# Optimization experiments

Measured on AMD Instinct MI355X. Metric: run time of the kernel, lower is better.

Reference implementation:

```python
import jax, jax.numpy as jnp
import numpy as np

N_SU = 8
DATA_DIM = N_SU * N_SU - 1  # 63
BATCH = 1048576


def _gell_mann(n):
    """Generalized Gell-Mann matrices of su(n), Tr(L_a L_b) = 2 delta_ab."""
    mats = []
    for j in range(n):
        for k in range(j + 1, n):
            m = np.zeros((n, n), dtype=np.complex128); m[j, k] = 1.0; m[k, j] = 1.0
            mats.append(m)
            m = np.zeros((n, n), dtype=np.complex128); m[j, k] = -1.0j; m[k, j] = 1.0j
            mats.append(m)
    for l in range(1, n):
        m = np.zeros((n, n), dtype=np.complex128)
        c = np.sqrt(2.0 / (l * (l + 1)))
        for j in range(l):
            m[j, j] = c
        m[l, l] = -l * c
        mats.append(m)
    return np.stack(mats)


def _structure_const(n):
    """f_abc = Tr([L_a,L_b]L_c)/(4i), d_abc = Tr({L_a,L_b}L_c)/4 (both real)."""
    L = _gell_mann(n)                                  # (D, n, n)
    P = np.einsum('aij,bjk->abik', L, L)               # L_a L_b
    comm = P - P.transpose(1, 0, 2, 3)
    anti = P + P.transpose(1, 0, 2, 3)
    f = (np.einsum('abik,cki->abc', comm, L) / 4.0j).real
    d = (np.einsum('abik,cki->abc', anti, L) / 4.0).real
    return f.astype(np.float32), d.astype(np.float32)

F_CONST, D_CONST = _structure_const(N_SU)              # (D, D, D) each, compile-time constants
TRI = np.stack(np.triu_indices(DATA_DIM, 0))           # incl. diagonal
TRI1 = np.stack(np.triu_indices(DATA_DIM, 1))          # strict upper


def setup_inputs() -> dict:
    key = jax.random.key(0)
    k1, k2, k3, k4, k5 = jax.random.split(key, 5)
    D = DATA_DIM
    return {
        'x': jax.random.normal(k1, (BATCH, D), dtype=jnp.float32),
        'r_x': jax.random.uniform(k2, (D * (D + 1) // 2,), dtype=jnp.float32),
        'r_y': jax.random.uniform(k3, (D * (D - 1) // 2,), dtype=jnp.float32),
        'N': jax.random.uniform(k4, (1,), dtype=jnp.float32),
        'omega': jax.random.uniform(k5, (D,), dtype=jnp.float32),
    }


def _forward(x, r_x, r_y, N, omega):
    f = jnp.asarray(F_CONST)
    d = jnp.asarray(D_CONST)
    D = DATA_DIM
    # NOTE: faithful to the torch source, where `v_x = v_y = torch.zeros(...)`
    # aliases ONE tensor: r_y overwrites r_x on the strict upper triangle and
    # v_x is v_y, which makes c_im exactly zero.
    v = jnp.zeros((D, D), dtype=x.dtype)
    v = v.at[TRI[0], TRI[1]].set(r_x)
    v = v.at[TRI1[0], TRI1[1]].set(r_y)
    v_x = v
    v_y = v
    c_re = v_x.T @ v_x + v_y.T @ v_y                   # einsum('ki,kj->ij', v, v) x2
    c_re = c_re / jnp.trace(c_re)
    c_im = v_x.T @ v_y - v_y.T @ v_x                   # exactly zero (aliasing)
    c_re = N * c_re

    # Precompute the small (D,D) superoperator coefficient matrices once, then
    # apply them to the batch with plain matmuls (bn,mn->bm).
    A1 = jnp.einsum('mjk,ij->mik', f, c_re)
    M_re1 = jnp.einsum('mik,nik->mn', A1, f)           # 'mjk,nik,ij->mn'
    A2 = jnp.einsum('mik,ij->mjk', f, c_re)
    M_re2 = jnp.einsum('mjk,njk->mn', A2, f)           # 'mik,njk,ij->mn'
    B1 = jnp.einsum('mjk,ij->mik', f, c_im)
    M_im1 = jnp.einsum('mik,nik->mn', B1, d)
    B2 = jnp.einsum('mik,ij->mjk', f, c_im)
    M_im2 = jnp.einsum('mjk,njk->mn', B2, d)
    M = -2.0 * M_re1 - 2.0 * M_re2 - 2.0 * M_im1 + 2.0 * M_im2

    d_super_x = x @ M.T                                 # (B, D)
    H = 8.0 * jnp.einsum('kij,k->ij', f, omega)
    h_commutator_x = x @ H.T                            # 'kij,k,bj->bi'
    tr_id = -8.0 * jnp.einsum('imj,ij->m', f, c_im)     # (D,), zero here

    S_x = h_commutator_x + d_super_x
    T_x = x + tr_id
    L_x = S_x + T_x
    return x + 0.01 * L_x


def reference(x, r_x, r_y, N, omega):
    return _forward(x, r_x, r_y, N, omega)
```

## Files before the change

### kernel.cpp

```cpp
#include <hip/hip_runtime.h>
#include <hip/hip_bf16.h>

#define DD 63
#define DD2 (DD * DD)
#define NSU 8

typedef __attribute__((ext_vector_type(8))) short short8;
typedef __attribute__((ext_vector_type(4))) float f32x4;

__device__ float  g_F[DD2 * DD];
__device__ float  g_B[DD * DD2];
__device__ float  g_cc[DD2];
__device__ float  g_scale;
__device__ unsigned short g_Gb[64 * 64];

__device__ __forceinline__ unsigned short f2bf(float f) {
    union { float f; unsigned u; } v; v.f = f;
    unsigned r = v.u + 0x7FFFu + ((v.u >> 16) & 1u);
    return (unsigned short)(r >> 16);
}

__device__ __forceinline__ void fill_L(int a, float (*re)[NSU], float (*im)[NSU]) {
    if (a < 56) {
        int p = a >> 1;
        int j = 0, rem = p;
        while (rem >= 7 - j) { rem -= 7 - j; ++j; }
        int k = j + 1 + rem;
        if ((a & 1) == 0) { re[j][k] = 1.f; re[k][j] = 1.f; }
        else             { im[j][k] = -1.f; im[k][j] = 1.f; }
    } else {
        int l = a - 55;
        float c = sqrtf(2.f / (float)(l * (l + 1)));
        for (int j = 0; j < l; ++j) re[j][j] = c;
        re[l][l] = -(float)l * c;
    }
}

__global__ __launch_bounds__(256) void setup_kernel(const float* __restrict__ r_x,
                                                    const float* __restrict__ r_y,
                                                    const float* __restrict__ Np) {
    const int t = threadIdx.x;
    if (blockIdx.x < DD) {
        const int a = blockIdx.x;
        __shared__ float Ar[NSU][NSU], Ai[NSU][NSU];
        __shared__ float Br[4][NSU][NSU], Bi[4][NSU][NSU];
        __shared__ float Cr[4][NSU][NSU], Ci[4][NSU][NSU];
        const int w = t >> 6, lane = t & 63;
        const int r = lane >> 3, c = lane & 7;
        if (t < 64) { Ar[r][c] = 0.f; Ai[r][c] = 0.f; }
        __syncthreads();
        if (t == 0) fill_L(a, Ar, Ai);
        __syncthreads();
        for (int rb = 0; rb < 16; ++rb) {
            const int b = rb * 4 + w;
            const bool act = (b < DD);
            if (act) { Br[w][r][c] = 0.f; Bi[w][r][c] = 0.f; }
            __syncthreads();
            if (act && lane == 0) fill_L(b, Br[w], Bi[w]);
            __syncthreads();
            if (act) {
                float pr = 0.f, pi = 0.f, qr = 0.f, qi = 0.f;
                #pragma unroll
                for (int k = 0; k < NSU; ++k) {
                    pr += Ar[r][k] * Br[w][k][c] - Ai[r][k] * Bi[w][k][c];
                    pi += Ar[r][k] * Bi[w][k][c] + Ai[r][k] * Br[w][k][c];
                    qr += Br[w][r][k] * Ar[k][c] - Bi[w][r][k] * Ai[k][c];
                    qi += Br[w][r][k] * Ai[k][c] + Bi[w][r][k] * Ar[k][c];
                }
                Cr[w][r][c] = pr - qr;
                Ci[w][r][c] = pi - qi;
            }
            __syncthreads();
            if (act && lane < DD) {
                float im;
                if (lane < 56) {
                    int p = lane >> 1;
                    int j = 0, rem = p;
                    while (rem >= 7 - j) { rem -= 7 - j; ++j; }
                    int k = j + 1 + rem;
                    if ((lane & 1) == 0) im = Ci[w][j][k] + Ci[w][k][j];
                    else                 im = Cr[w][j][k] - Cr[w][k][j];
                } else {
                    int l = lane - 55;
                    float cd = sqrtf(2.f / (float)(l * (l + 1)));
                    float s = 0.f;
                    for (int j = 0; j < l; ++j) s += Ci[w][j][j];
                    im = cd * s - (float)l * cd * Ci[w][l][l];
                }
                g_F[(a * DD + b) * DD + lane] = 0.25f * im;
            }
            __syncthreads();
        }
    } else {
        __shared__ float v[DD2];
        __shared__ float ccs[DD2];
        for (int idx = t; idx < DD2; idx += 256) {
            int i = idx / DD, j = idx % DD;
            float val = 0.f;
            if (j > i)       val = r_y[62 * i - (i * (i - 1)) / 2 + (j - i - 1)];
            else if (j == i) val = r_x[63 * i - (i * (i - 1)) / 2];
            v[idx] = val;
        }
        __syncthreads();
        for (int idx = t; idx < DD2; idx += 256) {
            int i = idx / DD, j = idx % DD;
            float s = 0.f;
            for (int k = 0; k < DD; ++k) s = fmaf(v[k * DD + i], v[k * DD + j], s);
            ccs[idx] = s;
            g_cc[idx] = s;
        }
        __syncthreads();
        if (t == 0) {
            float tr = 0.f;
            for (int i = 0; i < DD; ++i) tr += ccs[i * DD + i];
            g_scale = Np[0] / tr;
        }
    }
}

__global__ __launch_bounds__(256) void buildB_kernel() {
    __shared__ float scc[DD2];
    __shared__ float sf[DD2];
    const int t = threadIdx.x;
    const int n = blockIdx.x;
    for (int idx = t; idx < DD2; idx += 256) {
        scc[idx] = g_cc[idx];
        sf[idx]  = g_F[n * DD2 + idx];
    }
    __syncthreads();
    for (int idx = t; idx < DD2; idx += 256) {
        const int j = idx / DD, k = idx % DD;
        float s = 0.f;
        for (int i = 0; i < DD; ++i) s = fmaf(scc[i * DD + j], sf[i * DD + k], s);
        g_B[n * DD2 + idx] = s;
    }
}

__global__ __launch_bounds__(64) void buildKt_kernel(const float* __restrict__ omega) {
    const int m = blockIdx.x >> 6;
    const int n = blockIdx.x & 63;
    const int lane = threadIdx.x;
    if (m >= DD || n >= DD) {
        if (lane == 0) g_Gb[m * 64 + n] = 0;
        return;
    }
    const float* __restrict__ Fm = g_F + m * DD2;
    const float* __restrict__ Bn = g_B + n * DD2;
    float p = 0.f;
    for (int idx = lane; idx < DD2; idx += 64) p = fmaf(Fm[idx], Bn[idx], p);
    float h = (lane < DD) ? g_F[lane * DD2 + m * DD + n] * omega[lane] : 0.f;
    #pragma unroll
    for (int off = 32; off > 0; off >>= 1) {
        p += __shfl_down(p, off);
        h += __shfl_down(h, off);
    }
    if (lane == 0)
        g_Gb[m * 64 + n] = f2bf(0.01f * (-4.f * g_scale * p + 8.f * h)
                                + ((m == n) ? 1.01f : 0.f));
}

__global__ __launch_bounds__(256) void apply_kernel(const float* __restrict__ x,
                                                    float* __restrict__ out,
                                                    int ntiles, int nwaves) {
    __shared__ float slab[4][16 * 64];
    const int t = threadIdx.x;
    const int w = t >> 6, lane = t & 63;
    const int mrow = lane & 15, q = lane >> 4;
    float* __restrict__ S = slab[w];

    const short8* __restrict__ gG = (const short8*)g_Gb;
    short8 bfrag[2][4];
    #pragma unroll
    for (int kt = 0; kt < 2; ++kt)
        #pragma unroll
        for (int nt = 0; nt < 4; ++nt)
            bfrag[kt][nt] = gG[(nt * 16 + mrow) * 8 + kt * 4 + q];

    if (lane < 16) S[lane * 64 + (((15 ^ lane) << 2) | 3)] = 0.f;

    int soff[4][4];
    #pragma unroll
    for (int i = 0; i < 4; ++i) {
        const int f = i * 64 + lane;
        #pragma unroll
        for (int j = 0; j < 4; ++j) {
            const int e = 4 * f + j;
            const int r = e / 63, c = e - r * 63;
            soff[i][j] = r * 64 + ((((c >> 2) ^ r) << 2) | (c & 3));
        }
    }
    const bool act3 = (lane < 60);

    int tile = blockIdx.x * 4 + w;
    if (tile >= ntiles) return;

    float4 ld[4];
    {
        const float4* __restrict__ gp = (const float4*)(x + (size_t)tile * (16 * DD));
        ld[0] = gp[lane]; ld[1] = gp[lane + 64]; ld[2] = gp[lane + 128];
        if (act3) ld[3] = gp[lane + 192];
    }

    while (true) {
        #pragma unroll
        for (int i = 0; i < 3; ++i) {
            S[soff[i][0]] = ld[i].x; S[soff[i][1]] = ld[i].y;
            S[soff[i][2]] = ld[i].z; S[soff[i][3]] = ld[i].w;
        }
        if (act3) {
            S[soff[3][0]] = ld[3].x; S[soff[3][1]] = ld[3].y;
            S[soff[3][2]] = ld[3].z; S[soff[3][3]] = ld[3].w;
        }
        const size_t tb = (size_t)tile * (16 * DD);
        const int next = tile + nwaves;

        float va[2][8];
        #pragma unroll
        for (int kt = 0; kt < 2; ++kt) {
            const int c0 = 8 * kt + 2 * q;
            *(float4*)&va[kt][0] = *(const float4*)&S[mrow * 64 + (((c0    ) ^ mrow) << 2)];
            *(float4*)&va[kt][4] = *(const float4*)&S[mrow * 64 + (((c0 + 1) ^ mrow) << 2)];
        }

        if (next < ntiles) {
            const float4* __restrict__ gp = (const float4*)(x + (size_t)next * (16 * DD));
            ld[0] = gp[lane]; ld[1] = gp[lane + 64]; ld[2] = gp[lane + 128];
            if (act3) ld[3] = gp[lane + 192];
        }

        short8 af[2];
        #pragma unroll
        for (int kt = 0; kt < 2; ++kt)
            #pragma unroll
            for (int j = 0; j < 8; ++j) {
                __hip_bfloat16 h = __float2bfloat16(va[kt][j]);
                af[kt][j] = *reinterpret_cast<short*>(&h);
            }

        f32x4 acc[4] = {{0.f,0.f,0.f,0.f},{0.f,0.f,0.f,0.f},
                        {0.f,0.f,0.f,0.f},{0.f,0.f,0.f,0.f}};
        #pragma unroll
        for (int nt = 0; nt < 4; ++nt) {
            acc[nt] = __builtin_amdgcn_mfma_f32_16x16x32_bf16(af[0], bfrag[0][nt], acc[nt], 0, 0, 0);
            acc[nt] = __builtin_amdgcn_mfma_f32_16x16x32_bf16(af[1], bfrag[1][nt], acc[nt], 0, 0, 0);
        }

        #pragma unroll
        for (int nt = 0; nt < 4; ++nt) {
            const int ocol = nt * 16 + mrow;
            if (ocol < DD) {
                #pragma unroll
                for (int r = 0; r < 4; ++r) {
                    const int orow = q * 4 + r;
                    S[orow * 64 + ((((ocol >> 2) ^ orow) << 2) | (ocol & 3))] = acc[nt][r];
                }
            }
        }

        #pragma unroll
        for (int i = 0; i < 3; ++i) {
            float4 o;
            o.x = S[soff[i][0]]; o.y = S[soff[i][1]];
            o.z = S[soff[i][2]]; o.w = S[soff[i][3]];
            ((float4*)(out + tb))[i * 64 + lane] = o;
        }
        if (act3) {
            float4 o;
            o.x = S[soff[3][0]]; o.y = S[soff[3][1]];
            o.z = S[soff[3][2]]; o.w = S[soff[3][3]];
            ((float4*)(out + tb))[192 + lane] = o;
        }

        if (next >= ntiles) break;
        tile = next;
    }
}

extern "C" void kernel_launch(void* const* d_in, const int* in_sizes, int n_in,
                              void* d_out, int out_size, void* d_ws, size_t ws_size,
                              hipStream_t stream) {
    const float* x     = (const float*)d_in[0];
    const float* r_x   = (const float*)d_in[1];
    const float* r_y   = (const float*)d_in[2];
    const float* Np    = (const float*)d_in[3];
    const float* omega = (const float*)d_in[4];
    float* out = (float*)d_out;

    const int rows = in_sizes[0] / DD;
    const int ntiles = rows / 16;
    const int ablocks = 2048;
    const int nwaves = ablocks * 4;

    setup_kernel<<<DD + 1, 256, 0, stream>>>(r_x, r_y, Np);
    buildB_kernel<<<DD, 256, 0, stream>>>();
    buildKt_kernel<<<64 * 64, 64, 0, stream>>>(omega);
    apply_kernel<<<ablocks, 256, 0, stream>>>(x, out, ntiles, nwaves);
}
```

Before: 180.3 us.

## Parallelize setup over (a,b) pairs and double-buffer x prefetch in apply

Splits the setup kernel so each structure-constant pair (a,b) and each column of the c matrix gets its own small block, instead of 64 blocks looping serially. The global trace/scale is now recomputed inside buildKt from the diagonal of g_cc, which removes a serial reduction step. The apply kernel keeps two register tile buffers so it prefetches two tiles ahead, giving more loads in flight at the cost of extra registers. Note that the diagonal read uses g_cc[lane*64], which matches i*63+i only because the row stride is 63 and 64 = 63+1.

```diff
diff --git a/kernel.cpp b/kernel.cpp
--- a/kernel.cpp
+++ b/kernel.cpp
@@ -11,7 +11,6 @@
 __device__ float  g_F[DD2 * DD];
 __device__ float  g_B[DD * DD2];
 __device__ float  g_cc[DD2];
-__device__ float  g_scale;
 __device__ unsigned short g_Gb[64 * 64];
 
 __device__ __forceinline__ unsigned short f2bf(float f) {
@@ -36,84 +35,63 @@
     }
 }
 
-__global__ __launch_bounds__(256) void setup_kernel(const float* __restrict__ r_x,
-                                                    const float* __restrict__ r_y,
-                                                    const float* __restrict__ Np) {
+__global__ __launch_bounds__(64) void setup1_kernel(const float* __restrict__ r_x,
+                                                    const float* __restrict__ r_y) {
     const int t = threadIdx.x;
-    if (blockIdx.x < DD) {
-        const int a = blockIdx.x;
-        __shared__ float Ar[NSU][NSU], Ai[NSU][NSU];
-        __shared__ float Br[4][NSU][NSU], Bi[4][NSU][NSU];
-        __shared__ float Cr[4][NSU][NSU], Ci[4][NSU][NSU];
-        const int w = t >> 6, lane = t & 63;
-        const int r = lane >> 3, c = lane & 7;
-        if (t < 64) { Ar[r][c] = 0.f; Ai[r][c] = 0.f; }
+    if (blockIdx.x < DD2) {
+        __shared__ float Ar[NSU][NSU], Ai[NSU][NSU], Br[NSU][NSU], Bi[NSU][NSU];
+        __shared__ float Cr[NSU][NSU], Ci[NSU][NSU];
+        const int a = blockIdx.x / DD, b = blockIdx.x % DD;
+        const int r = t >> 3, c = t & 7;
+        Ar[r][c] = 0.f; Ai[r][c] = 0.f; Br[r][c] = 0.f; Bi[r][c] = 0.f;
         __syncthreads();
         if (t == 0) fill_L(a, Ar, Ai);
-        __syncthreads();
-        for (int rb = 0; rb < 16; ++rb) {
-            const int b = rb * 4 + w;
-            const bool act = (b < DD);
-            if (act) { Br[w][r][c] = 0.f; Bi[w][r][c] = 0.f; }
-            __syncthreads();
-            if (act && lane == 0) fill_L(b, Br[w], Bi[w]);
-            __syncthreads();
-            if (act) {
-                float pr = 0.f, pi = 0.f, qr = 0.f, qi = 0.f;
-                #pragma unroll
-                for (int k = 0; k < NSU; ++k) {
-                    pr += Ar[r][k] * Br[w][k][c] - Ai[r][k] * Bi[w][k][c];
-                    pi += Ar[r][k] * Bi[w][k][c] + Ai[r][k] * Br[w][k][c];
-                    qr += Br[w][r][k] * Ar[k][c] - Bi[w][r][k] * Ai[k][c];
-                    qi += Br[w][r][k] * Ai[k][c] + Bi[w][r][k] * Ar[k][c];
-                }
-                Cr[w][r][c] = pr - qr;
-                Ci[w][r][c] = pi - qi;
+        if (t == 1) fill_L(b, Br, Bi);
+        __syncthreads();
+        float pr = 0.f, pi = 0.f, qr = 0.f, qi = 0.f;
+        #pragma unroll
+        for (int k = 0; k < NSU; ++k) {
+            pr += Ar[r][k] * Br[k][c] - Ai[r][k] * Bi[k][c];
+            pi += Ar[r][k] * Bi[k][c] + Ai[r][k] * Br[k][c];
+            qr += Br[r][k] * Ar[k][c] - Bi[r][k] * Ai[k][c];
+            qi += Br[r][k] * Ai[k][c] + Bi[r][k] * Ar[k][c];
+        }
+        Cr[r][c] = pr - qr;
+        Ci[r][c] = pi - qi;
+        __syncthreads();
+        if (t < DD) {
+            float im;
+            if (t < 56) {
+                int p = t >> 1;
+                int j = 0, rem = p;
+                while (rem >= 7 - j) { rem -= 7 - j; ++j; }
+                int k = j + 1 + rem;
+                if ((t & 1) == 0) im = Ci[j][k] + Ci[k][j];
+                else              im = Cr[j][k] - Cr[k][j];
+            } else {
+                int l = t - 55;
+                float cd = sqrtf(2.f / (float)(l * (l + 1)));
+                float s = 0.f;
+                for (int j = 0; j < l; ++j) s += Ci[j][j];
+                im = cd * s - (float)l * cd * Ci[l][l];
             }
-            __syncthreads();
-            if (act && lane < DD) {
-                float im;
-                if (lane < 56) {
-                    int p = lane >> 1;
-                    int j = 0, rem = p;
-                    while (rem >= 7 - j) { rem -= 7 - j; ++j; }
-                    int k = j + 1 + rem;
-                    if ((lane & 1) == 0) im = Ci[w][j][k] + Ci[w][k][j];
-                    else                 im = Cr[w][j][k] - Cr[w][k][j];
-                } else {
-                    int l = lane - 55;
-                    float cd = sqrtf(2.f / (float)(l * (l + 1)));
-                    float s = 0.f;
-                    for (int j = 0; j < l; ++j) s += Ci[w][j][j];
-                    im = cd * s - (float)l * cd * Ci[w][l][l];
-                }
-                g_F[(a * DD + b) * DD + lane] = 0.25f * im;
-            }
-            __syncthreads();
+            g_F[(a * DD + b) * DD + t] = 0.25f * im;
         }
     } else {
         __shared__ float v[DD2];
-        __shared__ float ccs[DD2];
-        for (int idx = t; idx < DD2; idx += 256) {
-            int i = idx / DD, j = idx % DD;
+        const int jcol = blockIdx.x - DD2;
+        for (int idx = t; idx < DD2; idx += 64) {
+            int i = idx / DD, j = idx - i * DD;
             float val = 0.f;
             if (j > i)       val = r_y[62 * i - (i * (i - 1)) / 2 + (j - i - 1)];
             else if (j == i) val = r_x[63 * i - (i * (i - 1)) / 2];
             v[idx] = val;
         }
         __syncthreads();
-        for (int idx = t; idx < DD2; idx += 256) {
-            int i = idx / DD, j = idx % DD;
+        if (t < DD) {
             float s = 0.f;
-            for (int k = 0; k < DD; ++k) s = fmaf(v[k * DD + i], v[k * DD + j], s);
-            ccs[idx] = s;
-            g_cc[idx] = s;
-        }
-        __syncthreads();
-        if (t == 0) {
-            float tr = 0.f;
-            for (int i = 0; i < DD; ++i) tr += ccs[i * DD + i];
-            g_scale = Np[0] / tr;
+            for (int k = 0; k < DD; ++k) s = fmaf(v[k * DD + t], v[k * DD + jcol], s);
+            g_cc[t * DD + jcol] = s;
         }
     }
 }
@@ -136,7 +114,8 @@
     }
 }
 
-__global__ __launch_bounds__(64) void buildKt_kernel(const float* __restrict__ omega) {
+__global__ __launch_bounds__(64) void buildKt_kernel(const float* __restrict__ omega,
+                                                     const float* __restrict__ Np) {
     const int m = blockIdx.x >> 6;
     const int n = blockIdx.x & 63;
     const int lane = threadIdx.x;
@@ -144,6 +123,11 @@
         if (lane == 0) g_Gb[m * 64 + n] = 0;
         return;
     }
+    float d = (lane < DD) ? g_cc[lane * 64] : 0.f;
+    #pragma unroll
+    for (int off = 32; off > 0; off >>= 1) d += __shfl_xor(d, off);
+    const float scale = Np[0] / d;
+
     const float* __restrict__ Fm = g_F + m * DD2;
     const float* __restrict__ Bn = g_B + n * DD2;
     float p = 0.f;
@@ -155,7 +139,7 @@
         h += __shfl_down(h, off);
     }
     if (lane == 0)
-        g_Gb[m * 64 + n] = f2bf(0.01f * (-4.f * g_scale * p + 8.f * h)
+        g_Gb[m * 64 + n] = f2bf(0.01f * (-4.f * scale * p + 8.f * h)
                                 + ((m == n) ? 1.01f : 0.f));
 }
 
@@ -191,17 +175,13 @@
     }
     const bool act3 = (lane < 60);
 
-    int tile = blockIdx.x * 4 + w;
-    if (tile >= ntiles) return;
-
-    float4 ld[4];
-    {
-        const float4* __restrict__ gp = (const float4*)(x + (size_t)tile * (16 * DD));
+    auto load_tile = [&](float4 (&ld)[4], int tl) {
+        const float4* __restrict__ gp = (const float4*)(x + (size_t)tl * (16 * DD));
         ld[0] = gp[lane]; ld[1] = gp[lane + 64]; ld[2] = gp[lane + 128];
         if (act3) ld[3] = gp[lane + 192];
-    }
-
-    while (true) {
+    };
+
+    auto process = [&](float4 (&ld)[4], int cur, int pf) {
         #pragma unroll
         for (int i = 0; i < 3; ++i) {
             S[soff[i][0]] = ld[i].x; S[soff[i][1]] = ld[i].y;
@@ -211,9 +191,6 @@
             S[soff[3][0]] = ld[3].x; S[soff[3][1]] = ld[3].y;
             S[soff[3][2]] = ld[3].z; S[soff[3][3]] = ld[3].w;
         }
-        const size_t tb = (size_t)tile * (16 * DD);
-        const int next = tile + nwaves;
-
         float va[2][8];
         #pragma unroll
         for (int kt = 0; kt < 2; ++kt) {
@@ -221,12 +198,7 @@
             *(float4*)&va[kt][0] = *(const float4*)&S[mrow * 64 + (((c0    ) ^ mrow) << 2)];
             *(float4*)&va[kt][4] = *(const float4*)&S[mrow * 64 + (((c0 + 1) ^ mrow) << 2)];
         }
-
-        if (next < ntiles) {
-            const float4* __restrict__ gp = (const float4*)(x + (size_t)next * (16 * DD));
-            ld[0] = gp[lane]; ld[1] = gp[lane + 64]; ld[2] = gp[lane + 128];
-            if (act3) ld[3] = gp[lane + 192];
-        }
+        if (pf < ntiles) load_tile(ld, pf);
 
         short8 af[2];
         #pragma unroll
@@ -257,6 +229,7 @@
             }
         }
 
+        const size_t tb = (size_t)cur * (16 * DD);
         #pragma unroll
         for (int i = 0; i < 3; ++i) {
             float4 o;
@@ -270,9 +243,22 @@
             o.z = S[soff[3][2]]; o.w = S[soff[3][3]];
             ((float4*)(out + tb))[192 + lane] = o;
         }
-
-        if (next >= ntiles) break;
-        tile = next;
+    };
+
+    int tile = blockIdx.x * 4 + w;
+    if (tile >= ntiles) return;
+
+    float4 ldA[4], ldB[4];
+    load_tile(ldA, tile);
+    if (tile + nwaves < ntiles) load_tile(ldB, tile + nwaves);
+
+    for (;;) {
+        process(ldA, tile, tile + 2 * nwaves);
+        tile += nwaves;
+        if (tile >= ntiles) break;
+        process(ldB, tile, tile + 2 * nwaves);
+        tile += nwaves;
+        if (tile >= ntiles) break;
     }
 }
 
@@ -291,8 +277,8 @@
     const int ablocks = 2048;
     const int nwaves = ablocks * 4;
 
-    setup_kernel<<<DD + 1, 256, 0, stream>>>(r_x, r_y, Np);
+    setup1_kernel<<<DD2 + DD, 64, 0, stream>>>(r_x, r_y);
     buildB_kernel<<<DD, 256, 0, stream>>>();
-    buildKt_kernel<<<64 * 64, 64, 0, stream>>>(omega);
+    buildKt_kernel<<<64 * 64, 64, 0, stream>>>(omega, Np);
     apply_kernel<<<ablocks, 256, 0, stream>>>(x, out, ntiles, nwaves);
 }
```

New measurement: 185.0 us. +2.6%, slower.

## Fuse setup, buildB and buildKt into one cooperative kernel with grid syncs

Applied to the files above, without the earlier changes.

Replaces three separate small precompute kernel launches with a single cooperative kernel of 256 blocks that uses grid-wide syncs between stages. The work is also spread more widely: the F tensor is computed over 249 blocks instead of 63, the cc Gram matrix over 4 blocks, B over 252 blocks, and the trace scale is recomputed per block instead of stored globally. The aim is to remove launch gaps and improve parallelism in the serial setup chain, at the cost of grid-sync overhead and the cooperative launch requirements.

```diff
diff --git a/kernel.cpp b/kernel.cpp
--- a/kernel.cpp
+++ b/kernel.cpp
@@ -1,5 +1,8 @@
 #include <hip/hip_runtime.h>
 #include <hip/hip_bf16.h>
+#include <hip/hip_cooperative_groups.h>
+
+namespace cg = cooperative_groups;
 
 #define DD 63
 #define DD2 (DD * DD)
@@ -11,7 +14,6 @@
 __device__ float  g_F[DD2 * DD];
 __device__ float  g_B[DD * DD2];
 __device__ float  g_cc[DD2];
-__device__ float  g_scale;
 __device__ unsigned short g_Gb[64 * 64];
 
 __device__ __forceinline__ unsigned short f2bf(float f) {
@@ -36,39 +38,42 @@
     }
 }
 
-__global__ __launch_bounds__(256) void setup_kernel(const float* __restrict__ r_x,
+__global__ __launch_bounds__(256) void chain_kernel(const float* __restrict__ r_x,
                                                     const float* __restrict__ r_y,
-                                                    const float* __restrict__ Np) {
+                                                    const float* __restrict__ Np,
+                                                    const float* __restrict__ omega) {
     const int t = threadIdx.x;
-    if (blockIdx.x < DD) {
-        const int a = blockIdx.x;
-        __shared__ float Ar[NSU][NSU], Ai[NSU][NSU];
-        __shared__ float Br[4][NSU][NSU], Bi[4][NSU][NSU];
-        __shared__ float Cr[4][NSU][NSU], Ci[4][NSU][NSU];
-        const int w = t >> 6, lane = t & 63;
-        const int r = lane >> 3, c = lane & 7;
-        if (t < 64) { Ar[r][c] = 0.f; Ai[r][c] = 0.f; }
-        __syncthreads();
-        if (t == 0) fill_L(a, Ar, Ai);
-        __syncthreads();
-        for (int rb = 0; rb < 16; ++rb) {
-            const int b = rb * 4 + w;
-            const bool act = (b < DD);
-            if (act) { Br[w][r][c] = 0.f; Bi[w][r][c] = 0.f; }
+    const int bid = blockIdx.x;
+    const int w = t >> 6, lane = t & 63;
+
+    __shared__ float Ar[4][NSU][NSU], Ai[4][NSU][NSU], Br[4][NSU][NSU], Bi[4][NSU][NSU];
+    __shared__ float Cr[4][NSU][NSU], Ci[4][NSU][NSU];
+    __shared__ float buf1[DD2];
+    __shared__ float buf2[DD2];
+
+    if (bid < 249) {
+        const int rr = lane >> 3, c = lane & 7;
+        for (int r = 0; r < 4; ++r) {
+            const int u = bid * 16 + r * 4 + w;
+            const bool act = (u < DD2);
+            int a = 0, b = 0;
+            if (act) { a = u / DD; b = u % DD; }
+            if (act) { Ar[w][rr][c] = 0.f; Ai[w][rr][c] = 0.f; Br[w][rr][c] = 0.f; Bi[w][rr][c] = 0.f; }
             __syncthreads();
-            if (act && lane == 0) fill_L(b, Br[w], Bi[w]);
+            if (act && lane == 0) fill_L(a, Ar[w], Ai[w]);
+            if (act && lane == 1) fill_L(b, Br[w], Bi[w]);
             __syncthreads();
             if (act) {
                 float pr = 0.f, pi = 0.f, qr = 0.f, qi = 0.f;
                 #pragma unroll
                 for (int k = 0; k < NSU; ++k) {
-                    pr += Ar[r][k] * Br[w][k][c] - Ai[r][k] * Bi[w][k][c];
-                    pi += Ar[r][k] * Bi[w][k][c] + Ai[r][k] * Br[w][k][c];
-                    qr += Br[w][r][k] * Ar[k][c] - Bi[w][r][k] * Ai[k][c];
-                    qi += Br[w][r][k] * Ai[k][c] + Bi[w][r][k] * Ar[k][c];
+                    pr += Ar[w][rr][k] * Br[w][k][c] - Ai[w][rr][k] * Bi[w][k][c];
+                    pi += Ar[w][rr][k] * Bi[w][k][c] + Ai[w][rr][k] * Br[w][k][c];
+                    qr += Br[w][rr][k] * Ar[w][k][c] - Bi[w][rr][k] * Ai[w][k][c];
+                    qi += Br[w][rr][k] * Ai[w][k][c] + Bi[w][rr][k] * Ar[w][k][c];
                 }
-                Cr[w][r][c] = pr - qr;
-                Ci[w][r][c] = pi - qi;
+                Cr[w][rr][c] = pr - qr;
+                Ci[w][rr][c] = pi - qi;
             }
             __syncthreads();
             if (act && lane < DD) {
@@ -91,72 +96,76 @@
             }
             __syncthreads();
         }
-    } else {
-        __shared__ float v[DD2];
-        __shared__ float ccs[DD2];
+    } else if (bid >= 252) {
         for (int idx = t; idx < DD2; idx += 256) {
-            int i = idx / DD, j = idx % DD;
+            int i = idx / DD, j = idx - i * DD;
             float val = 0.f;
             if (j > i)       val = r_y[62 * i - (i * (i - 1)) / 2 + (j - i - 1)];
             else if (j == i) val = r_x[63 * i - (i * (i - 1)) / 2];
-            v[idx] = val;
+            buf1[idx] = val;
         }
         __syncthreads();
+        const int cb = bid - 252;
+        for (int e = t; e < 63 * 16; e += 256) {
+            const int i = e % 63;
+            const int j = cb * 16 + e / 63;
+            if (j < DD) {
+                float s = 0.f;
+                for (int k = 0; k < DD; ++k) s = fmaf(buf1[k * DD + i], buf1[k * DD + j], s);
+                g_cc[i * DD + j] = s;
+            }
+        }
+    }
+
+    cg::this_grid().sync();
+
+    if (bid < 252) {
+        const int n = bid >> 2, qt = bid & 3;
         for (int idx = t; idx < DD2; idx += 256) {
-            int i = idx / DD, j = idx % DD;
+            buf2[idx] = g_cc[idx];
+            buf1[idx] = g_F[n * DD2 + idx];
+        }
+        __syncthreads();
+        const int lo = qt * 993;
+        const int hi = (qt == 3) ? DD2 : (qt + 1) * 993;
+        for (int idx = lo + t; idx < hi; idx += 256) {
+            const int j = idx / DD, k = idx - j * DD;
             float s = 0.f;
-            for (int k = 0; k < DD; ++k) s = fmaf(v[k * DD + i], v[k * DD + j], s);
-            ccs[idx] = s;
-            g_cc[idx] = s;
-        }
-        __syncthreads();
-        if (t == 0) {
-            float tr = 0.f;
-            for (int i = 0; i < DD; ++i) tr += ccs[i * DD + i];
-            g_scale = Np[0] / tr;
-        }
-    }
-}
-
-__global__ __launch_bounds__(256) void buildB_kernel() {
-    __shared__ float scc[DD2];
-    __shared__ float sf[DD2];
-    const int t = threadIdx.x;
-    const int n = blockIdx.x;
-    for (int idx = t; idx < DD2; idx += 256) {
-        scc[idx] = g_cc[idx];
-        sf[idx]  = g_F[n * DD2 + idx];
-    }
-    __syncthreads();
-    for (int idx = t; idx < DD2; idx += 256) {
-        const int j = idx / DD, k = idx % DD;
-        float s = 0.f;
-        for (int i = 0; i < DD; ++i) s = fmaf(scc[i * DD + j], sf[i * DD + k], s);
-        g_B[n * DD2 + idx] = s;
-    }
-}
-
-__global__ __launch_bounds__(64) void buildKt_kernel(const float* __restrict__ omega) {
-    const int m = blockIdx.x >> 6;
-    const int n = blockIdx.x & 63;
-    const int lane = threadIdx.x;
-    if (m >= DD || n >= DD) {
-        if (lane == 0) g_Gb[m * 64 + n] = 0;
-        return;
-    }
-    const float* __restrict__ Fm = g_F + m * DD2;
-    const float* __restrict__ Bn = g_B + n * DD2;
-    float p = 0.f;
-    for (int idx = lane; idx < DD2; idx += 64) p = fmaf(Fm[idx], Bn[idx], p);
-    float h = (lane < DD) ? g_F[lane * DD2 + m * DD + n] * omega[lane] : 0.f;
-    #pragma unroll
-    for (int off = 32; off > 0; off >>= 1) {
-        p += __shfl_down(p, off);
-        h += __shfl_down(h, off);
-    }
-    if (lane == 0)
-        g_Gb[m * 64 + n] = f2bf(0.01f * (-4.f * g_scale * p + 8.f * h)
-                                + ((m == n) ? 1.01f : 0.f));
+            for (int i = 0; i < DD; ++i) s = fmaf(buf2[i * DD + j], buf1[i * DD + k], s);
+            g_B[n * DD2 + idx] = s;
+        }
+    }
+
+    cg::this_grid().sync();
+
+    {
+        float d = (lane < DD) ? g_cc[lane * 64] : 0.f;
+        #pragma unroll
+        for (int off = 32; off > 0; off >>= 1) d += __shfl_xor(d, off);
+        const float scale = Np[0] / d;
+
+        for (int r = 0; r < 4; ++r) {
+            const int u = bid * 4 + w + r * 1024;
+            const int m = u >> 6, n = u & 63;
+            if (m >= DD || n >= DD) {
+                if (lane == 0) g_Gb[m * 64 + n] = 0;
+                continue;
+            }
+            const float* __restrict__ Fm = g_F + m * DD2;
+            const float* __restrict__ Bn = g_B + n * DD2;
+            float p = 0.f;
+            for (int idx = lane; idx < DD2; idx += 64) p = fmaf(Fm[idx], Bn[idx], p);
+            float h = (lane < DD) ? g_F[lane * DD2 + m * DD + n] * omega[lane] : 0.f;
+            #pragma unroll
+            for (int off = 32; off > 0; off >>= 1) {
+                p += __shfl_down(p, off);
+                h += __shfl_down(h, off);
+            }
+            if (lane == 0)
+                g_Gb[m * 64 + n] = f2bf(0.01f * (-4.f * scale * p + 8.f * h)
+                                        + ((m == n) ? 1.01f : 0.f));
+        }
+    }
 }
 
 __global__ __launch_bounds__(256) void apply_kernel(const float* __restrict__ x,
@@ -291,8 +300,8 @@
     const int ablocks = 2048;
     const int nwaves = ablocks * 4;
 
-    setup_kernel<<<DD + 1, 256, 0, stream>>>(r_x, r_y, Np);
-    buildB_kernel<<<DD, 256, 0, stream>>>();
-    buildKt_kernel<<<64 * 64, 64, 0, stream>>>(omega);
+    void* args[] = { (void*)&r_x, (void*)&r_y, (void*)&Np, (void*)&omega };
+    hipLaunchCooperativeKernel((const void*)chain_kernel, dim3(256), dim3(256),
+                               args, 0, stream);
     apply_kernel<<<ablocks, 256, 0, stream>>>(x, out, ntiles, nwaves);
 }
```

Measured after the change: 232.3 us. 1.29x slower.
